# Kernel optimization log

Measured on AMD Instinct MI355X. Metric: run time of the kernel, lower is better.

Reference implementation:

```python
import jax, jax.numpy as jnp
import numpy as np

H, L = 3, 2  # heads, layers
B, S, D = 16, 512, 512  # batch, seq_len, mem_dim


def setup_inputs() -> dict:
    key = jax.random.key(0)
    ks = jax.random.split(key, 6)
    scale = 0.02
    return {
        "adj_list": jax.random.uniform(ks[0], (H, B, S, S), dtype=jnp.float32),
        "gcn_inputs": jax.random.normal(ks[1], (B, S, D), dtype=jnp.float32),
        "mask": jnp.zeros((B, S), dtype=bool),
        "domain_mask": jnp.zeros((B, S), dtype=bool),
        "W_gcn": jax.random.normal(ks[2], (H * L, D, D), dtype=jnp.float32) * scale,
        "b_gcn": jnp.zeros((H * L, D), dtype=jnp.float32),
        "W_out": jax.random.normal(ks[3], (D, H * L * D), dtype=jnp.float32) * scale,
        "b_out": jnp.zeros((D,), dtype=jnp.float32),
    }


def reference(adj_list, gcn_inputs, mask, domain_mask, W_gcn, b_gcn, W_out, b_out):
    # mask/domain_mask are unused by the original forward; dropout is identity (eval).
    head_outs = []
    for i in range(H):
        adj = adj_list[i]                              # [B,S,S]
        denom = adj.sum(2, keepdims=True) + 1.0        # [B,S,1]
        outputs = gcn_inputs
        layer_outs = []
        for l in range(L):
            idx = i * L + l
            Ax = jnp.einsum('bst,btd->bsd', adj, outputs)
            # Linear(Ax) + Linear(outputs) == (Ax + outputs) @ W.T + 2*b
            AxW = jnp.einsum('bsd,ed->bse', Ax + outputs, W_gcn[idx]) + 2.0 * b_gcn[idx]
            outputs = jax.nn.relu(AxW / denom)
            layer_outs.append(outputs)
        head_outs.append(jnp.concatenate(layer_outs, axis=2))  # [B,S,L*D]
    final = jnp.concatenate(head_outs, axis=2)                  # [B,S,H*L*D]
    out = jnp.einsum('bsf,df->bsd', final, W_out) + b_out
    return gcn_inputs + out
```

## Files before the change

### kernel.cpp

```cpp
#include <hip/hip_runtime.h>
#include <hip/hip_bf16.h>
#include <stdint.h>


#define HH 3
#define LL 2
#define BB 16
#define SS 512
#define DD 512
#define FF 3072

typedef __attribute__((ext_vector_type(8))) short bf16x8;
typedef __attribute__((ext_vector_type(4))) float f32x4;
typedef __attribute__((ext_vector_type(4))) float vfloat4;
typedef __attribute__((ext_vector_type(4))) short shortx4;
typedef __attribute__((ext_vector_type(2))) unsigned int uint2v;

__device__ __forceinline__ short f2b(float x) {
  union { float f; uint32_t u; } v; v.f = x;
  return (short)((v.u + 0x7FFFu + ((v.u >> 16) & 1u)) >> 16);
}
__device__ __forceinline__ float b2f(short s) {
  union { uint32_t u; float f; } v; v.u = ((uint32_t)(uint16_t)s) << 16;
  return v.f;
}
__device__ __forceinline__ float c8(uint8_t b) {
  return __builtin_amdgcn_cvt_f32_fp8((int)b, 0);
}

__device__ __forceinline__ void gld16b(const uint8_t* g, uint8_t* l) {
  __builtin_amdgcn_global_load_lds((const __attribute__((address_space(1))) void*)g,
                                   (__attribute__((address_space(3))) void*)l, 16, 0, 0);
}

__device__ __forceinline__ int xswz(int grid) {
  int cpx = grid >> 3;
  return (blockIdx.x & 7) * cpx + (blockIdx.x >> 3);
}

__global__ void k_prep(const float* __restrict__ adj, uint8_t* __restrict__ adjf8,
                       float* __restrict__ rden,
                       const float* __restrict__ wg, const float* __restrict__ wo,
                       uint8_t* __restrict__ wgb, uint8_t* __restrict__ wob,
                       const float* __restrict__ x, uint8_t* __restrict__ xt,
                       short* __restrict__ x0b) {
  __shared__ short t[64][72];
  int bid = blockIdx.x;
  int tid = threadIdx.x;
  if (bid < 6144) {
    int row = bid * 4 + (tid >> 6);
    int lane = tid & 63;
    const float* src = adj + (size_t)row * SS;
    vfloat4 a = *(const vfloat4*)(src + lane * 8);
    vfloat4 b = *(const vfloat4*)(src + lane * 8 + 4);
    uint32_t w0 = 0, w1 = 0;
    w0 = __builtin_amdgcn_cvt_pk_fp8_f32(a[0], a[1], w0, false);
    w0 = __builtin_amdgcn_cvt_pk_fp8_f32(a[2], a[3], w0, true);
    w1 = __builtin_amdgcn_cvt_pk_fp8_f32(b[0], b[1], w1, false);
    w1 = __builtin_amdgcn_cvt_pk_fp8_f32(b[2], b[3], w1, true);
    uint2v o; o[0] = w0; o[1] = w1;
    *(uint2v*)(adjf8 + (size_t)row * SS + lane * 8) = o;
    float s = a[0]+a[1]+a[2]+a[3]+b[0]+b[1]+b[2]+b[3];
    #pragma unroll
    for (int off = 32; off > 0; off >>= 1) s += __shfl_xor(s, off);
    if (lane == 0) rden[row] = 1.0f / (s + 1.0f);
  } else if (bid < 6912) {
    size_t i = ((size_t)(bid - 6144) * 256 + tid) * 8;
    vfloat4 a = *(const vfloat4*)(wg + i);
    vfloat4 b = *(const vfloat4*)(wg + i + 4);
    uint32_t w0 = 0, w1 = 0;
    w0 = __builtin_amdgcn_cvt_pk_fp8_f32(a[0]*64.f, a[1]*64.f, w0, false);
    w0 = __builtin_amdgcn_cvt_pk_fp8_f32(a[2]*64.f, a[3]*64.f, w0, true);
    w1 = __builtin_amdgcn_cvt_pk_fp8_f32(b[0]*64.f, b[1]*64.f, w1, false);
    w1 = __builtin_amdgcn_cvt_pk_fp8_f32(b[2]*64.f, b[3]*64.f, w1, true);
    uint2v o; o[0] = w0; o[1] = w1;
    *(uint2v*)(wgb + i) = o;
    a = *(const vfloat4*)(wo + i);
    b = *(const vfloat4*)(wo + i + 4);
    w0 = 0; w1 = 0;
    w0 = __builtin_amdgcn_cvt_pk_fp8_f32(a[0]*64.f, a[1]*64.f, w0, false);
    w0 = __builtin_amdgcn_cvt_pk_fp8_f32(a[2]*64.f, a[3]*64.f, w0, true);
    w1 = __builtin_amdgcn_cvt_pk_fp8_f32(b[0]*64.f, b[1]*64.f, w1, false);
    w1 = __builtin_amdgcn_cvt_pk_fp8_f32(b[2]*64.f, b[3]*64.f, w1, true);
    o[0] = w0; o[1] = w1;
    *(uint2v*)(wob + i) = o;
  } else {
    int bid2 = bid - 6912;
    int b = bid2 >> 6, q = bid2 & 63;
    int s0 = (q >> 3) * 64, d0 = (q & 7) * 64;
    int r = tid >> 4, c4 = (tid & 15) * 4;
    const float* src = x + ((size_t)b * SS + s0) * DD + d0;
    #pragma unroll
    for (int rr = 0; rr < 64; rr += 16) {
      vfloat4 v = *(const vfloat4*)(src + (size_t)(r + rr) * DD + c4);
      shortx4 o4;
      o4[0] = f2b(v[0]); o4[1] = f2b(v[1]); o4[2] = f2b(v[2]); o4[3] = f2b(v[3]);
      t[r+rr][c4+0] = o4[0]; t[r+rr][c4+1] = o4[1];
      t[r+rr][c4+2] = o4[2]; t[r+rr][c4+3] = o4[3];
      *(shortx4*)(x0b + ((size_t)b * SS + s0 + r + rr) * DD + d0 + c4) = o4;
    }
    __syncthreads();
    int dloc = tid >> 3, s8 = (tid & 7) * 8;
    uint8_t* dst = xt + (size_t)b * DD * SS + s0;
    #pragma unroll
    for (int dd = 0; dd < 64; dd += 32) {
      float f[8];
      #pragma unroll
      for (int j = 0; j < 8; j++) f[j] = b2f(t[s8 + j][dloc + dd]);
      uint32_t w0 = 0, w1 = 0;
      w0 = __builtin_amdgcn_cvt_pk_fp8_f32(f[0], f[1], w0, false);
      w0 = __builtin_amdgcn_cvt_pk_fp8_f32(f[2], f[3], w0, true);
      w1 = __builtin_amdgcn_cvt_pk_fp8_f32(f[4], f[5], w1, false);
      w1 = __builtin_amdgcn_cvt_pk_fp8_f32(f[6], f[7], w1, true);
      uint2v o; o[0] = w0; o[1] = w1;
      *(uint2v*)(dst + (size_t)(d0 + dloc + dd) * SS + s8) = o;
    }
  }
}

__device__ __forceinline__ void compute32f8(const uint8_t* As, const uint8_t* Bs,
                                            int wr, int wc, int lrow, int kslot,
                                            f32x4 acc[4][4]) {
  long af[4], bv[4];
  #pragma unroll
  for (int m = 0; m < 4; m++)
    af[m] = *(const long*)(As + (wr*64 + m*16 + lrow) * 32 + kslot);
  #pragma unroll
  for (int n = 0; n < 4; n++)
    bv[n] = *(const long*)(Bs + (wc*64 + n*16 + lrow) * 32 + kslot);
  #pragma unroll
  for (int m = 0; m < 4; m++)
    #pragma unroll
    for (int n = 0; n < 4; n++)
      acc[m][n] = __builtin_amdgcn_mfma_f32_16x16x32_fp8_fp8(af[m], bv[n], acc[m][n], 0, 0, 0);
}

__device__ __forceinline__ void gemmf8(const uint8_t* __restrict__ A, int lda,
                                       const uint8_t* __restrict__ Bm, int ldb,
                                       int K, uint8_t* lds, f32x4 acc[4][4]) {
  int tid = threadIdx.x;
  int lane = tid & 63, wid = tid >> 6;
  int wr = wid >> 1, wc = wid & 1;
  int lrow = lane & 15;
  int kslot = (((lane >> 4) ^ ((((lane & 15) >> 2) & 1) << 1)) << 3);
  int row = tid >> 1, h = tid & 1;
  int gc = ((h ^ ((row >> 2) & 1)) << 4);
  const uint8_t* ga = A + (size_t)row * lda + gc;
  const uint8_t* gb = Bm + (size_t)row * ldb + gc;

  #define STG(BUF, kt) do { \
    gld16b(ga + (size_t)(kt) * 32, (BUF) + tid * 16); \
    gld16b(gb + (size_t)(kt) * 32, (BUF) + 4096 + tid * 16); } while (0)
  #define STEPW(VM) do { \
    asm volatile("s_waitcnt vmcnt(" #VM ")" ::: "memory"); \
    __builtin_amdgcn_s_barrier(); \
    __builtin_amdgcn_sched_barrier(0); } while (0)
  #define ROT4 do { uint8_t* t_ = p0; p0 = p1; p1 = p2; p2 = p3; p3 = t_; } while (0)

  uint8_t* p0 = lds;
  uint8_t* p1 = lds + 8192;
  uint8_t* p2 = lds + 16384;
  uint8_t* p3 = lds + 24576;
  int NT = K / 32;
  STG(p0, 0); STG(p1, 1); STG(p2, 2);
  for (int t = 0; t < NT - 3; t++) {
    STEPW(4);
    STG(p3, t + 3);
    compute32f8(p0, p0 + 4096, wr, wc, lrow, kslot, acc);
    ROT4;
  }
  STEPW(4); compute32f8(p0, p0 + 4096, wr, wc, lrow, kslot, acc); ROT4;
  STEPW(2); compute32f8(p0, p0 + 4096, wr, wc, lrow, kslot, acc); ROT4;
  STEPW(0); compute32f8(p0, p0 + 4096, wr, wc, lrow, kslot, acc);
  #undef STG
  #undef STEPW
  #undef ROT4
}

__global__ __launch_bounds__(256, 4) void k_gemmA(
    const uint8_t* __restrict__ adjf8, const uint8_t* __restrict__ btp,
    const short* __restrict__ x0b, const uint8_t* __restrict__ finb,
    int layer, uint8_t* __restrict__ axpx) {
  __shared__ uint8_t lds[32768];
  int bx = xswz(HH*BB*16);
  int q = bx & 15;
  int g = bx >> 4;
  int b = g / 3, h = g - b * 3;
  int hb = h * BB + b;
  int tr = q >> 2, tc = q & 3;
  const uint8_t* A = adjf8 + (size_t)hb * SS * SS + (size_t)(tr * 128) * SS;
  const uint8_t* Bm = (layer == 0)
      ? btp + (size_t)b * DD * SS + (size_t)(tc * 128) * SS
      : btp + (size_t)hb * DD * SS + (size_t)(tc * 128) * SS;
  f32x4 acc[4][4];
  #pragma unroll
  for (int m = 0; m < 4; m++)
    #pragma unroll
    for (int n = 0; n < 4; n++) acc[m][n] = (f32x4){0.f, 0.f, 0.f, 0.f};
  gemmf8(A, SS, Bm, SS, SS, lds, acc);
  int lane = threadIdx.x & 63, wid = threadIdx.x >> 6;
  int wr = wid >> 1, wc = wid & 1;
  int r4 = (lane >> 4) * 4, cn = lane & 15;
  uint8_t* outp = axpx + (size_t)hb * SS * DD;
  #pragma unroll
  for (int m = 0; m < 4; m++) {
    #pragma unroll
    for (int n = 0; n < 4; n++) {
      int sb = tr*128 + wr*64 + m*16 + r4;
      int d = tc*128 + wc*64 + n*16 + cn;
      float vv[4];
      #pragma unroll
      for (int r = 0; r < 4; r++) {
        float v;
        if (layer == 0)
          v = acc[m][n][r] + b2f(x0b[((size_t)b * SS + sb + r) * DD + d]);
        else
          v = (acc[m][n][r] + c8(finb[((size_t)b * SS + sb + r) * FF + (size_t)(h * LL) * DD + d]))
              * 0.015625f;
        vv[r] = v * 2.0f;
      }
      uint32_t pk4 = 0;
      pk4 = __builtin_amdgcn_cvt_pk_fp8_f32(vv[0], vv[1], pk4, false);
      pk4 = __builtin_amdgcn_cvt_pk_fp8_f32(vv[2], vv[3], pk4, true);
      #pragma unroll
      for (int r = 0; r < 4; r++)
        outp[(size_t)(sb + r) * DD + d] = (uint8_t)(pk4 >> (8 * r));
    }
  }
}

__global__ __launch_bounds__(256, 4) void k_gemmB(
    const uint8_t* __restrict__ axpx, const uint8_t* __restrict__ wgb,
    const float* __restrict__ bg, const float* __restrict__ rden,
    int layer, uint8_t* __restrict__ finb, uint8_t* __restrict__ yt) {
  __shared__ uint8_t lds[32768];
  int bx = xswz(HH*BB*16);
  int hb = bx >> 4, q = bx & 15;
  int h = hb / BB, b = hb % BB;
  int tr = q >> 2, tc = q & 3;
  int idx = h * LL + layer;
  const uint8_t* A = axpx + (size_t)hb * SS * DD + (size_t)(tr * 128) * DD;
  const uint8_t* Bm = wgb + (size_t)idx * DD * DD + (size_t)(tc * 128) * DD;
  f32x4 acc[4][4];
  #pragma unroll
  for (int m = 0; m < 4; m++)
    #pragma unroll
    for (int n = 0; n < 4; n++) acc[m][n] = (f32x4){0.f, 0.f, 0.f, 0.f};
  gemmf8(A, DD, Bm, DD, DD, lds, acc);
  int lane = threadIdx.x & 63, wid = threadIdx.x >> 6;
  int wr = wid >> 1, wc = wid & 1;
  int r4 = (lane >> 4) * 4, cn = lane & 15;
  #pragma unroll
  for (int m = 0; m < 4; m++) {
    #pragma unroll
    for (int n = 0; n < 4; n++) {
      int sb = tr*128 + wr*64 + m*16 + r4;
      int e = tc*128 + wc*64 + n*16 + cn;
      float vv[4];
      #pragma unroll
      for (int r = 0; r < 4; r++) {
        float v = (acc[m][n][r] * 0.0078125f + 2.0f * bg[(size_t)idx * DD + e])
                  * rden[(size_t)hb * SS + sb + r];
        vv[r] = fmaxf(v, 0.0f) * 64.0f;
      }
      uint32_t pk4 = 0;
      pk4 = __builtin_amdgcn_cvt_pk_fp8_f32(vv[0], vv[1], pk4, false);
      pk4 = __builtin_amdgcn_cvt_pk_fp8_f32(vv[2], vv[3], pk4, true);
      #pragma unroll
      for (int r = 0; r < 4; r++)
        finb[((size_t)b * SS + sb + r) * FF + (size_t)idx * DD + e] =
            (uint8_t)(pk4 >> (8 * r));
      if (layer == 0)
        *(uint32_t*)(yt + (size_t)hb * DD * SS + (size_t)e * SS + sb) = pk4;
    }
  }
}

__global__ __launch_bounds__(256, 4) void k_gemmF(
    const uint8_t* __restrict__ finb, const uint8_t* __restrict__ wob,
    short* __restrict__ part) {
  __shared__ uint8_t lds[32768];
  int bx = xswz(BB*16*2);
  int ks = bx >> 8;
  int q = bx & 255;
  int tr = q >> 2, tc = q & 3;
  const uint8_t* A = finb + (size_t)(tr * 128) * FF + ks * 1536;
  const uint8_t* Bm = wob + (size_t)(tc * 128) * FF + ks * 1536;
  f32x4 acc[4][4];
  #pragma unroll
  for (int m = 0; m < 4; m++)
    #pragma unroll
    for (int n = 0; n < 4; n++) acc[m][n] = (f32x4){0.f, 0.f, 0.f, 0.f};
  gemmf8(A, FF, Bm, FF, 1536, lds, acc);
  int lane = threadIdx.x & 63, wid = threadIdx.x >> 6;
  int wr = wid >> 1, wc = wid & 1;
  int r4 = (lane >> 4) * 4, cn = lane & 15;
  short* op = part + (size_t)ks * ((size_t)BB*SS*DD);
  #pragma unroll
  for (int m = 0; m < 4; m++) {
    #pragma unroll
    for (int n = 0; n < 4; n++) {
      #pragma unroll
      for (int r = 0; r < 4; r++) {
        int row = tr*128 + wr*64 + m*16 + r4 + r;
        int d = tc*128 + wc*64 + n*16 + cn;
        op[(size_t)row * DD + d] = f2b(acc[m][n][r] * (1.0f / 4096.0f));
      }
    }
  }
}

__global__ void k_redF(const short* __restrict__ part, const float* __restrict__ x0f,
                       const float* __restrict__ bo, float* __restrict__ out) {
  const size_t PSZ = (size_t)BB * SS * DD;
  size_t i = ((size_t)blockIdx.x * 256 + threadIdx.x) * 8;
  if (i >= PSZ) return;
  int d = (int)(i & (DD - 1));
  bf16x8 q0 = *(const bf16x8*)(part + i);
  bf16x8 q1 = *(const bf16x8*)(part + PSZ + i);
  vfloat4 xa = *(const vfloat4*)(x0f + i);
  vfloat4 xb = *(const vfloat4*)(x0f + i + 4);
  vfloat4 ba = *(const vfloat4*)(bo + d);
  vfloat4 bb = *(const vfloat4*)(bo + d + 4);
  vfloat4 oa, ob;
  #pragma unroll
  for (int j = 0; j < 4; j++) {
    oa[j] = b2f(q0[j]) + b2f(q1[j]) + xa[j] + ba[j];
    ob[j] = b2f(q0[j+4]) + b2f(q1[j+4]) + xb[j] + bb[j];
  }
  *(vfloat4*)(out + i) = oa;
  *(vfloat4*)(out + i + 4) = ob;
}

extern "C" void kernel_launch(void* const* d_in, const int* in_sizes, int n_in,
                              void* d_out, int out_size, void* d_ws, size_t ws_size,
                              hipStream_t stream) {
  const float* adj = (const float*)d_in[0];
  const float* x0  = (const float*)d_in[1];
  const float* wg  = (const float*)d_in[4];
  const float* bg  = (const float*)d_in[5];
  const float* wo  = (const float*)d_in[6];
  const float* bo  = (const float*)d_in[7];
  float* out = (float*)d_out;

  char* p = (char*)d_ws;
  uint8_t* adjf8 = (uint8_t*)p; p += (size_t)HH*BB*SS*SS;
  uint8_t* x0t   = (uint8_t*)p; p += (size_t)BB*DD*SS;
  uint8_t* yt    = (uint8_t*)p; p += (size_t)HH*BB*DD*SS;
  uint8_t* axpx  = (uint8_t*)p; p += (size_t)HH*BB*SS*DD;
  uint8_t* finb  = (uint8_t*)p; p += (size_t)BB*SS*FF;
  uint8_t* wgb   = (uint8_t*)p; p += (size_t)HH*LL*DD*DD;
  uint8_t* wob   = (uint8_t*)p; p += (size_t)DD*FF;
  float*   rden  = (float*)p;   p += (size_t)HH*BB*SS*4;
  short*   x0b   = (short*)p;   p += (size_t)BB*SS*DD*2;
  short* part = (short*)d_ws;

  k_prep<<<6144 + 768 + BB*64, 256, 0, stream>>>(
      adj, adjf8, rden, wg, wo, wgb, wob, x0, x0t, x0b);

  k_gemmA<<<HH*BB*16, 256, 0, stream>>>(adjf8, x0t, x0b, finb, 0, axpx);
  k_gemmB<<<HH*BB*16, 256, 0, stream>>>(axpx, wgb, bg, rden, 0, finb, yt);
  k_gemmA<<<HH*BB*16, 256, 0, stream>>>(adjf8, yt, x0b, finb, 1, axpx);
  k_gemmB<<<HH*BB*16, 256, 0, stream>>>(axpx, wgb, bg, rden, 1, finb, yt);
  k_gemmF<<<BB*16*2, 256, 0, stream>>>(finb, wob, part);
  k_redF<<<2048, 256, 0, stream>>>(part, x0, bo, out);
}
```

Baseline: 162.1 us.

## Switch FP8 GEMMs to 16x16x128 scaled MFMA with K=128 double-buffered tiles

Replaces the 16x16x32 FP8 MFMA with the MI355X 16x16x128 f8f6f4 scaled MFMA, using unit scales (0x7F). The shared GEMM core now stages 128-wide K tiles into 64KB of XOR-swizzled LDS with two buffers instead of a four-deep ring of 32-wide tiles. The aim is to cut instruction count and barrier overhead per unit of K. In exchange, occupancy drops (launch bounds go from 4 to 2 blocks), there is less pipelining depth, and each step waits for vmcnt(0).

```diff
diff --git a/kernel.cpp b/kernel.cpp
--- a/kernel.cpp
+++ b/kernel.cpp
@@ -15,6 +15,8 @@
 typedef __attribute__((ext_vector_type(4))) float vfloat4;
 typedef __attribute__((ext_vector_type(4))) short shortx4;
 typedef __attribute__((ext_vector_type(2))) unsigned int uint2v;
+typedef __attribute__((ext_vector_type(8))) int i32x8;
+typedef __attribute__((ext_vector_type(4))) int i32x4;
 
 __device__ __forceinline__ short f2b(float x) {
   union { float f; uint32_t u; } v; v.f = x;
@@ -118,70 +120,80 @@
   }
 }
 
-__device__ __forceinline__ void compute32f8(const uint8_t* As, const uint8_t* Bs,
-                                            int wr, int wc, int lrow, int kslot,
-                                            f32x4 acc[4][4]) {
-  long af[4], bv[4];
+__device__ __forceinline__ void compute128(const uint8_t* As, const uint8_t* Bs,
+                                           int wr, int wc, int lr, int lk,
+                                           f32x4 acc[4][4]) {
+  i32x8 af[4], bv[4];
+  #pragma unroll
+  for (int m = 0; m < 4; m++) {
+    int r = wr*64 + m*16 + lr;
+    const uint8_t* base = As + (size_t)r * 128;
+    int x = r & 7;
+    i32x4 lo = *(const i32x4*)(base + (((2*lk)     ^ x) << 4));
+    i32x4 hi = *(const i32x4*)(base + (((2*lk + 1) ^ x) << 4));
+    af[m] = (i32x8){lo[0], lo[1], lo[2], lo[3], hi[0], hi[1], hi[2], hi[3]};
+  }
+  #pragma unroll
+  for (int n = 0; n < 4; n++) {
+    int r = wc*64 + n*16 + lr;
+    const uint8_t* base = Bs + (size_t)r * 128;
+    int x = r & 7;
+    i32x4 lo = *(const i32x4*)(base + (((2*lk)     ^ x) << 4));
+    i32x4 hi = *(const i32x4*)(base + (((2*lk + 1) ^ x) << 4));
+    bv[n] = (i32x8){lo[0], lo[1], lo[2], lo[3], hi[0], hi[1], hi[2], hi[3]};
+  }
   #pragma unroll
   for (int m = 0; m < 4; m++)
-    af[m] = *(const long*)(As + (wr*64 + m*16 + lrow) * 32 + kslot);
-  #pragma unroll
-  for (int n = 0; n < 4; n++)
-    bv[n] = *(const long*)(Bs + (wc*64 + n*16 + lrow) * 32 + kslot);
-  #pragma unroll
-  for (int m = 0; m < 4; m++)
     #pragma unroll
     for (int n = 0; n < 4; n++)
-      acc[m][n] = __builtin_amdgcn_mfma_f32_16x16x32_fp8_fp8(af[m], bv[n], acc[m][n], 0, 0, 0);
-}
-
-__device__ __forceinline__ void gemmf8(const uint8_t* __restrict__ A, int lda,
+      acc[m][n] = __builtin_amdgcn_mfma_scale_f32_16x16x128_f8f6f4(
+          af[m], bv[n], acc[m][n], 0 , 0 ,
+          0, 0x7F , 0, 0x7F );
+}
+
+__device__ __forceinline__ void gemmx8(const uint8_t* __restrict__ A, int lda,
                                        const uint8_t* __restrict__ Bm, int ldb,
                                        int K, uint8_t* lds, f32x4 acc[4][4]) {
   int tid = threadIdx.x;
   int lane = tid & 63, wid = tid >> 6;
   int wr = wid >> 1, wc = wid & 1;
-  int lrow = lane & 15;
-  int kslot = (((lane >> 4) ^ ((((lane & 15) >> 2) & 1) << 1)) << 3);
-  int row = tid >> 1, h = tid & 1;
-  int gc = ((h ^ ((row >> 2) & 1)) << 4);
-  const uint8_t* ga = A + (size_t)row * lda + gc;
-  const uint8_t* gb = Bm + (size_t)row * ldb + gc;
+  int lr = lane & 15, lk = lane >> 4;
+  int sr = tid >> 3, ss = tid & 7;
+  int scol = ((ss ^ (sr & 7)) << 4);
+  const uint8_t* gA = A + (size_t)sr * lda + scol;
+  const uint8_t* gB = Bm + (size_t)sr * ldb + scol;
+  uint8_t* b0 = lds;
+  uint8_t* b1 = lds + 32768;
 
   #define STG(BUF, kt) do { \
-    gld16b(ga + (size_t)(kt) * 32, (BUF) + tid * 16); \
-    gld16b(gb + (size_t)(kt) * 32, (BUF) + 4096 + tid * 16); } while (0)
-  #define STEPW(VM) do { \
-    asm volatile("s_waitcnt vmcnt(" #VM ")" ::: "memory"); \
+    _Pragma("unroll") for (int i = 0; i < 4; i++) { \
+      gld16b(gA + (size_t)(kt) * 128 + (size_t)i * 32 * lda, (BUF) + tid * 16 + i * 4096); \
+      gld16b(gB + (size_t)(kt) * 128 + (size_t)i * 32 * ldb, (BUF) + 16384 + tid * 16 + i * 4096); \
+    } } while (0)
+  #define WAITB do { \
+    asm volatile("s_waitcnt vmcnt(0) lgkmcnt(0)" ::: "memory"); \
     __builtin_amdgcn_s_barrier(); \
     __builtin_amdgcn_sched_barrier(0); } while (0)
-  #define ROT4 do { uint8_t* t_ = p0; p0 = p1; p1 = p2; p2 = p3; p3 = t_; } while (0)
-
-  uint8_t* p0 = lds;
-  uint8_t* p1 = lds + 8192;
-  uint8_t* p2 = lds + 16384;
-  uint8_t* p3 = lds + 24576;
-  int NT = K / 32;
-  STG(p0, 0); STG(p1, 1); STG(p2, 2);
-  for (int t = 0; t < NT - 3; t++) {
-    STEPW(4);
-    STG(p3, t + 3);
-    compute32f8(p0, p0 + 4096, wr, wc, lrow, kslot, acc);
-    ROT4;
-  }
-  STEPW(4); compute32f8(p0, p0 + 4096, wr, wc, lrow, kslot, acc); ROT4;
-  STEPW(2); compute32f8(p0, p0 + 4096, wr, wc, lrow, kslot, acc); ROT4;
-  STEPW(0); compute32f8(p0, p0 + 4096, wr, wc, lrow, kslot, acc);
+
+  int NT = K >> 7;
+  STG(b0, 0);
+  for (int t = 0; t < NT; t += 2) {
+    WAITB;
+    STG(b1, t + 1);
+    compute128(b0, b0 + 16384, wr, wc, lr, lk, acc);
+    WAITB;
+    if (t + 2 < NT) STG(b0, t + 2);
+    compute128(b1, b1 + 16384, wr, wc, lr, lk, acc);
+  }
   #undef STG
-  #undef STEPW
-  #undef ROT4
-}
-
-__global__ __launch_bounds__(256, 4) void k_gemmA(
+  #undef WAITB
+}
+
+__global__ __launch_bounds__(256, 2) void k_gemmA(
     const uint8_t* __restrict__ adjf8, const uint8_t* __restrict__ btp,
     const short* __restrict__ x0b, const uint8_t* __restrict__ finb,
     int layer, uint8_t* __restrict__ axpx) {
-  __shared__ uint8_t lds[32768];
+  extern __shared__ uint8_t lds[];
   int bx = xswz(HH*BB*16);
   int q = bx & 15;
   int g = bx >> 4;
@@ -197,7 +209,7 @@
   for (int m = 0; m < 4; m++)
     #pragma unroll
     for (int n = 0; n < 4; n++) acc[m][n] = (f32x4){0.f, 0.f, 0.f, 0.f};
-  gemmf8(A, SS, Bm, SS, SS, lds, acc);
+  gemmx8(A, SS, Bm, SS, SS, lds, acc);
   int lane = threadIdx.x & 63, wid = threadIdx.x >> 6;
   int wr = wid >> 1, wc = wid & 1;
   int r4 = (lane >> 4) * 4, cn = lane & 15;
@@ -229,11 +241,11 @@
   }
 }
 
-__global__ __launch_bounds__(256, 4) void k_gemmB(
+__global__ __launch_bounds__(256, 2) void k_gemmB(
     const uint8_t* __restrict__ axpx, const uint8_t* __restrict__ wgb,
     const float* __restrict__ bg, const float* __restrict__ rden,
     int layer, uint8_t* __restrict__ finb, uint8_t* __restrict__ yt) {
-  __shared__ uint8_t lds[32768];
+  extern __shared__ uint8_t lds[];
   int bx = xswz(HH*BB*16);
   int hb = bx >> 4, q = bx & 15;
   int h = hb / BB, b = hb % BB;
@@ -246,7 +258,7 @@
   for (int m = 0; m < 4; m++)
     #pragma unroll
     for (int n = 0; n < 4; n++) acc[m][n] = (f32x4){0.f, 0.f, 0.f, 0.f};
-  gemmf8(A, DD, Bm, DD, DD, lds, acc);
+  gemmx8(A, DD, Bm, DD, DD, lds, acc);
   int lane = threadIdx.x & 63, wid = threadIdx.x >> 6;
   int wr = wid >> 1, wc = wid & 1;
   int r4 = (lane >> 4) * 4, cn = lane & 15;
@@ -276,10 +288,10 @@
   }
 }
 
-__global__ __launch_bounds__(256, 4) void k_gemmF(
+__global__ __launch_bounds__(256, 2) void k_gemmF(
     const uint8_t* __restrict__ finb, const uint8_t* __restrict__ wob,
     short* __restrict__ part) {
-  __shared__ uint8_t lds[32768];
+  extern __shared__ uint8_t lds[];
   int bx = xswz(BB*16*2);
   int ks = bx >> 8;
   int q = bx & 255;
@@ -291,7 +303,7 @@
   for (int m = 0; m < 4; m++)
     #pragma unroll
     for (int n = 0; n < 4; n++) acc[m][n] = (f32x4){0.f, 0.f, 0.f, 0.f};
-  gemmf8(A, FF, Bm, FF, 1536, lds, acc);
+  gemmx8(A, FF, Bm, FF, 1536, lds, acc);
   int lane = threadIdx.x & 63, wid = threadIdx.x >> 6;
   int wr = wid >> 1, wc = wid & 1;
   int r4 = (lane >> 4) * 4, cn = lane & 15;
@@ -355,13 +367,20 @@
   short*   x0b   = (short*)p;   p += (size_t)BB*SS*DD*2;
   short* part = (short*)d_ws;
 
+  hipFuncSetAttribute((const void*)k_gemmA,
+                      hipFuncAttributeMaxDynamicSharedMemorySize, 65536);
+  hipFuncSetAttribute((const void*)k_gemmB,
+                      hipFuncAttributeMaxDynamicSharedMemorySize, 65536);
+  hipFuncSetAttribute((const void*)k_gemmF,
+                      hipFuncAttributeMaxDynamicSharedMemorySize, 65536);
+
   k_prep<<<6144 + 768 + BB*64, 256, 0, stream>>>(
       adj, adjf8, rden, wg, wo, wgb, wob, x0, x0t, x0b);
 
-  k_gemmA<<<HH*BB*16, 256, 0, stream>>>(adjf8, x0t, x0b, finb, 0, axpx);
-  k_gemmB<<<HH*BB*16, 256, 0, stream>>>(axpx, wgb, bg, rden, 0, finb, yt);
-  k_gemmA<<<HH*BB*16, 256, 0, stream>>>(adjf8, yt, x0b, finb, 1, axpx);
-  k_gemmB<<<HH*BB*16, 256, 0, stream>>>(axpx, wgb, bg, rden, 1, finb, yt);
-  k_gemmF<<<BB*16*2, 256, 0, stream>>>(finb, wob, part);
+  k_gemmA<<<HH*BB*16, 256, 65536, stream>>>(adjf8, x0t, x0b, finb, 0, axpx);
+  k_gemmB<<<HH*BB*16, 256, 65536, stream>>>(axpx, wgb, bg, rden, 0, finb, yt);
+  k_gemmA<<<HH*BB*16, 256, 65536, stream>>>(adjf8, yt, x0b, finb, 1, axpx);
+  k_gemmB<<<HH*BB*16, 256, 65536, stream>>>(axpx, wgb, bg, rden, 1, finb, yt);
+  k_gemmF<<<BB*16*2, 256, 65536, stream>>>(finb, wob, part);
   k_redF<<<2048, 256, 0, stream>>>(part, x0, bo, out);
 }
```

Measured after the change: 202.4 us. +24.9%, slower.

## Widen FP8 GEMM K-step to 64 with triple-buffered LDS pipeline

Applied to the files above, without the earlier changes.

The shared FP8 GEMM core now stages 64-wide K tiles per iteration, with four 16-byte loads per thread and a new XOR swizzle, instead of 32-wide tiles. The pipeline goes from a 4-deep ring of 8 KB buffers to a 3-deep ring of 16 KB buffers. This halves the number of barriers and waitcnt steps per K loop and doubles the MFMA work between synchronizations. In exchange, LDS per block grows to 48 KB and launch bounds drop to 3 blocks per CU, which reduces occupancy and shortens the prefetch distance in tiles.

```diff
diff --git a/kernel.cpp b/kernel.cpp
--- a/kernel.cpp
+++ b/kernel.cpp
@@ -118,21 +118,25 @@
   }
 }
 
-__device__ __forceinline__ void compute32f8(const uint8_t* As, const uint8_t* Bs,
-                                            int wr, int wc, int lrow, int kslot,
-                                            f32x4 acc[4][4]) {
-  long af[4], bv[4];
-  #pragma unroll
-  for (int m = 0; m < 4; m++)
-    af[m] = *(const long*)(As + (wr*64 + m*16 + lrow) * 32 + kslot);
-  #pragma unroll
-  for (int n = 0; n < 4; n++)
-    bv[n] = *(const long*)(Bs + (wc*64 + n*16 + lrow) * 32 + kslot);
-  #pragma unroll
-  for (int m = 0; m < 4; m++)
+__device__ __forceinline__ void compute64f8(const uint8_t* As, const uint8_t* Bs,
+                                            int wr, int wc, int lr, int lk,
+                                            int sx, f32x4 acc[4][4]) {
+  #pragma unroll
+  for (int h = 0; h < 2; h++) {
+    int slot = ((((h << 1) + (lk >> 1)) ^ sx) << 4) + (lk & 1) * 8;
+    long af[4], bv[4];
+    #pragma unroll
+    for (int m = 0; m < 4; m++)
+      af[m] = *(const long*)(As + (size_t)(wr*64 + m*16 + lr) * 64 + slot);
     #pragma unroll
     for (int n = 0; n < 4; n++)
-      acc[m][n] = __builtin_amdgcn_mfma_f32_16x16x32_fp8_fp8(af[m], bv[n], acc[m][n], 0, 0, 0);
+      bv[n] = *(const long*)(Bs + (size_t)(wc*64 + n*16 + lr) * 64 + slot);
+    #pragma unroll
+    for (int m = 0; m < 4; m++)
+      #pragma unroll
+      for (int n = 0; n < 4; n++)
+        acc[m][n] = __builtin_amdgcn_mfma_f32_16x16x32_fp8_fp8(af[m], bv[n], acc[m][n], 0, 0, 0);
+  }
 }
 
 __device__ __forceinline__ void gemmf8(const uint8_t* __restrict__ A, int lda,
@@ -141,47 +145,49 @@
   int tid = threadIdx.x;
   int lane = tid & 63, wid = tid >> 6;
   int wr = wid >> 1, wc = wid & 1;
-  int lrow = lane & 15;
-  int kslot = (((lane >> 4) ^ ((((lane & 15) >> 2) & 1) << 1)) << 3);
-  int row = tid >> 1, h = tid & 1;
-  int gc = ((h ^ ((row >> 2) & 1)) << 4);
-  const uint8_t* ga = A + (size_t)row * lda + gc;
-  const uint8_t* gb = Bm + (size_t)row * ldb + gc;
+  int lr = lane & 15, lk = lane >> 4;
+  int sx = (lr ^ (lr >> 2)) & 3;
+  int sr = tid >> 2, ss = tid & 3;
+  int gc = ((ss ^ ((sr ^ (sr >> 2)) & 3)) << 4);
+  const uint8_t* gA = A + (size_t)sr * lda + gc;
+  const uint8_t* gB = Bm + (size_t)sr * ldb + gc;
 
   #define STG(BUF, kt) do { \
-    gld16b(ga + (size_t)(kt) * 32, (BUF) + tid * 16); \
-    gld16b(gb + (size_t)(kt) * 32, (BUF) + 4096 + tid * 16); } while (0)
+    gld16b(gA + (size_t)(kt) * 64,                        (BUF) + tid * 16); \
+    gld16b(gA + (size_t)(kt) * 64 + (size_t)64 * lda,     (BUF) + 4096 + tid * 16); \
+    gld16b(gB + (size_t)(kt) * 64,                        (BUF) + 8192 + tid * 16); \
+    gld16b(gB + (size_t)(kt) * 64 + (size_t)64 * ldb,     (BUF) + 12288 + tid * 16); \
+  } while (0)
   #define STEPW(VM) do { \
     asm volatile("s_waitcnt vmcnt(" #VM ")" ::: "memory"); \
     __builtin_amdgcn_s_barrier(); \
     __builtin_amdgcn_sched_barrier(0); } while (0)
-  #define ROT4 do { uint8_t* t_ = p0; p0 = p1; p1 = p2; p2 = p3; p3 = t_; } while (0)
+  #define ROT3 do { uint8_t* t_ = p0; p0 = p1; p1 = p2; p2 = t_; } while (0)
 
   uint8_t* p0 = lds;
-  uint8_t* p1 = lds + 8192;
-  uint8_t* p2 = lds + 16384;
-  uint8_t* p3 = lds + 24576;
-  int NT = K / 32;
-  STG(p0, 0); STG(p1, 1); STG(p2, 2);
-  for (int t = 0; t < NT - 3; t++) {
+  uint8_t* p1 = lds + 16384;
+  uint8_t* p2 = lds + 32768;
+  int NT = K >> 6;
+  STG(p0, 0);
+  STG(p1, 1);
+  for (int t = 0; t < NT - 2; t++) {
     STEPW(4);
-    STG(p3, t + 3);
-    compute32f8(p0, p0 + 4096, wr, wc, lrow, kslot, acc);
-    ROT4;
-  }
-  STEPW(4); compute32f8(p0, p0 + 4096, wr, wc, lrow, kslot, acc); ROT4;
-  STEPW(2); compute32f8(p0, p0 + 4096, wr, wc, lrow, kslot, acc); ROT4;
-  STEPW(0); compute32f8(p0, p0 + 4096, wr, wc, lrow, kslot, acc);
+    STG(p2, t + 2);
+    compute64f8(p0, p0 + 8192, wr, wc, lr, lk, sx, acc);
+    ROT3;
+  }
+  STEPW(4); compute64f8(p0, p0 + 8192, wr, wc, lr, lk, sx, acc); ROT3;
+  STEPW(0); compute64f8(p0, p0 + 8192, wr, wc, lr, lk, sx, acc);
   #undef STG
   #undef STEPW
-  #undef ROT4
-}
-
-__global__ __launch_bounds__(256, 4) void k_gemmA(
+  #undef ROT3
+}
+
+__global__ __launch_bounds__(256, 3) void k_gemmA(
     const uint8_t* __restrict__ adjf8, const uint8_t* __restrict__ btp,
     const short* __restrict__ x0b, const uint8_t* __restrict__ finb,
     int layer, uint8_t* __restrict__ axpx) {
-  __shared__ uint8_t lds[32768];
+  __shared__ uint8_t lds[49152];
   int bx = xswz(HH*BB*16);
   int q = bx & 15;
   int g = bx >> 4;
@@ -229,11 +235,11 @@
   }
 }
 
-__global__ __launch_bounds__(256, 4) void k_gemmB(
+__global__ __launch_bounds__(256, 3) void k_gemmB(
     const uint8_t* __restrict__ axpx, const uint8_t* __restrict__ wgb,
     const float* __restrict__ bg, const float* __restrict__ rden,
     int layer, uint8_t* __restrict__ finb, uint8_t* __restrict__ yt) {
-  __shared__ uint8_t lds[32768];
+  __shared__ uint8_t lds[49152];
   int bx = xswz(HH*BB*16);
   int hb = bx >> 4, q = bx & 15;
   int h = hb / BB, b = hb % BB;
@@ -276,10 +282,10 @@
   }
 }
 
-__global__ __launch_bounds__(256, 4) void k_gemmF(
+__global__ __launch_bounds__(256, 3) void k_gemmF(
     const uint8_t* __restrict__ finb, const uint8_t* __restrict__ wob,
     short* __restrict__ part) {
-  __shared__ uint8_t lds[32768];
+  __shared__ uint8_t lds[49152];
   int bx = xswz(BB*16*2);
   int ks = bx >> 8;
   int q = bx & 255;
```

New measurement: 139.5 us. 1.16x faster.
